# Performance work log

Measured on AMD Instinct MI355X. Metric: run time of the kernel, lower is better.

## Reference

```python
import jax, jax.numpy as jnp
import numpy as np

T, B, IN, H = 256, 128, 512, 1024


def setup_inputs() -> dict:
    key = jax.random.key(0)
    ks = jax.random.split(key, 13)
    s = 1.0 / float(np.sqrt(H))  # torch LSTMCell init: U(-1/sqrt(H), 1/sqrt(H))
    u = lambda k, shp: jax.random.uniform(k, shp, jnp.float32, -s, s)
    return {
        "x": jax.random.normal(ks[0], (T, B, IN), jnp.float32),
        "h0_fwd": jax.random.normal(ks[1], (B, H), jnp.float32),
        "c0_fwd": jax.random.normal(ks[2], (B, H), jnp.float32),
        "h0_rev": jax.random.normal(ks[3], (B, H), jnp.float32),
        "c0_rev": jax.random.normal(ks[4], (B, H), jnp.float32),
        "W_ih_f": u(ks[5], (4 * H, IN)),
        "W_hh_f": u(ks[6], (4 * H, H)),
        "b_ih_f": u(ks[7], (4 * H,)),
        "b_hh_f": u(ks[8], (4 * H,)),
        "W_ih_r": u(ks[9], (4 * H, IN)),
        "W_hh_r": u(ks[10], (4 * H, H)),
        "b_ih_r": u(ks[11], (4 * H,)),
        "b_hh_r": u(ks[12], (4 * H,)),
    }


def _lstm(x, h0, c0, Wih, Whh, bih, bhh, reverse):
    # Precompute the input projection for all timesteps in one big GEMM.
    xp = jnp.einsum('tbi,gi->tbg', x, Wih) + bih + bhh  # [T, B, 4H]

    def step(carry, xg):
        h, c = carry
        gates = xg + h @ Whh.T  # [B, 4H]
        i, f, g, o = jnp.split(gates, 4, axis=-1)  # torch gate order: i, f, g, o
        c = jax.nn.sigmoid(f) * c + jax.nn.sigmoid(i) * jnp.tanh(g)
        h = jax.nn.sigmoid(o) * jnp.tanh(c)
        return (h, c), h

    # reverse=True scans backward in time but emits outputs in original order,
    # exactly matching ReverseLSTMLayer's reverse-process-then-reverse-outputs.
    (h, c), ys = jax.lax.scan(step, (h0, c0), xp, reverse=reverse)
    return ys, h, c


def reference(x, h0_fwd, c0_fwd, h0_rev, c0_rev,
              W_ih_f, W_hh_f, b_ih_f, b_hh_f,
              W_ih_r, W_hh_r, b_ih_r, b_hh_r):
    yf, hf, cf = _lstm(x, h0_fwd, c0_fwd, W_ih_f, W_hh_f, b_ih_f, b_hh_f, False)
    yr, hr, cr = _lstm(x, h0_rev, c0_rev, W_ih_r, W_hh_r, b_ih_r, b_hh_r, True)
    out = jnp.concatenate([yf, yr], axis=-1)  # [T, B, 2H]
    # Faithful to the original's `hidden, cell = output_states` quirk:
    # `hidden` is the forward direction's (h, c) pair stacked,
    # `cell` is the reverse direction's (h, c) pair stacked.
    hidden = jnp.stack([hf, cf])  # [2, B, H]
    cell = jnp.stack([hr, cr])    # [2, B, H]
    return out, (hidden, cell)
```

## Files before the change

### kernel.cpp

```cpp
#include <hip/hip_runtime.h>
#include <hip/hip_bf16.h>

typedef unsigned short u16;
typedef __attribute__((ext_vector_type(8))) short bf16x8;
typedef __attribute__((ext_vector_type(8))) u16   u16x8;
typedef __attribute__((ext_vector_type(4))) float f32x4;

#define T_STEPS 256
#define BATCH   128
#define INDIM   512
#define HDIM    1024
#define GDIM    4096
#define KTOT    1536

#define OFF_XBF   ((size_t)0)
#define XBF_BYTES ((size_t)T_STEPS * BATCH * INDIM * 2)
#define OFF_BM    (OFF_XBF + XBF_BYTES)
#define BM_BYTES  ((size_t)2 * GDIM * KTOT * 2)
#define OFF_BIAS  (OFF_BM + BM_BYTES)
#define BIAS_BYTES ((size_t)2 * GDIM * 4)
#define OFF_CNT   (OFF_BIAS + BIAS_BYTES)
#define OFF_ROLL  (OFF_CNT + 8192)
#define ROLL_BYTES ((size_t)(T_STEPS + 1) * 2 * BATCH * HDIM * 2)
#define WS_NEED   (OFF_ROLL + ROLL_BYTES)


__device__ __forceinline__ u16 f2b(float f) {
  __hip_bfloat16 h = __float2bfloat16(f);
  return *reinterpret_cast<u16*>(&h);
}

__global__ void k_cast_x(const float* __restrict__ x, u16* __restrict__ xs) {
  int i = blockIdx.x * 256 + threadIdx.x;
  int t   = i >> 13;
  int r13 = i & 8191;
  int row = r13 >> 6;
  int c0  = (r13 & 63) * 8;
  int q = row >> 5, rloc = row & 31;
  int mi = rloc >> 4, ar = rloc & 15;
  int kq = c0 >> 7, kr = c0 & 127;
  int ks = kr >> 5, h4 = (kr & 31) >> 3;
  int lane = h4 * 16 + ar;
  const float* src = x + ((size_t)t * BATCH + row) * INDIM + c0;
  f32x4 a = *reinterpret_cast<const f32x4*>(src);
  f32x4 b = *reinterpret_cast<const f32x4*>(src + 4);
  u16x8 u;
  u[0] = f2b(a[0]); u[1] = f2b(a[1]); u[2] = f2b(a[2]); u[3] = f2b(a[3]);
  u[4] = f2b(b[0]); u[5] = f2b(b[1]); u[6] = f2b(b[2]); u[7] = f2b(b[3]);
  size_t dst = ((((((size_t)t * 4 + q) * 4 + kq) * 4 + ks) * 2 + mi) * 64 + lane) * 8;
  *reinterpret_cast<u16x8*>(xs + dst) = u;
}

__global__ void k_build_b(const float* __restrict__ Whh_f, const float* __restrict__ Wih_f,
                          const float* __restrict__ Whh_r, const float* __restrict__ Wih_r,
                          u16* __restrict__ Bm) {
  int blk = blockIdx.x;
  int dir = blk >> 5, jt = blk & 31;
  const float* Whh = dir ? Whh_r : Whh_f;
  const float* Wih = dir ? Wih_r : Wih_f;
  u16* dst = Bm + (size_t)blk * 128 * KTOT;
  for (int c = 0; c < 128; c++) {
    int G = (c >> 5) * HDIM + jt * 32 + (c & 31);
    for (int k = threadIdx.x; k < KTOT; k += 256) {
      float v = (k < HDIM) ? Whh[(size_t)G * HDIM + k] : Wih[(size_t)G * INDIM + (k - HDIM)];
      dst[c * KTOT + k] = f2b(v);
    }
  }
}

__global__ void k_init(const float* __restrict__ h0f, const float* __restrict__ h0r,
                       const float* __restrict__ bihf, const float* __restrict__ bhhf,
                       const float* __restrict__ bihr, const float* __restrict__ bhhr,
                       u16* __restrict__ hfrag, float* __restrict__ bias,
                       unsigned* __restrict__ flags) {
  int i = blockIdx.x * 256 + threadIdx.x;
  if (i < 2 * BATCH * HDIM) {
    int dir = i / (BATCH * HDIM);
    int rem = i - dir * BATCH * HDIM;
    int r = rem / HDIM, c = rem - r * HDIM;
    int q = r >> 5, rloc = r & 31;
    int mi = rloc >> 4, ar = rloc & 15;
    int kq = c >> 8, ks = (c >> 5) & 7, h4 = (c & 31) >> 3, e = c & 7;
    const float* h0 = dir ? h0r : h0f;
    size_t off = ((size_t)(dir * 4 + q)) * 32768
               + (((size_t)(kq * 8 + ks) * 2 + mi) * 64 + h4 * 16 + ar) * 8 + e;
    hfrag[off] = f2b(h0[rem]);
  }
  if (i < 2 * GDIM) {
    int dir = i / GDIM, g = i - dir * GDIM;
    bias[i] = dir ? (bihr[g] + bhhr[g]) : (bihf[g] + bhhf[g]);
  }
  if (i < 512) flags[i] = 0;
}

__global__ __launch_bounds__(512, 2) void k_lstm(
    const u16* __restrict__ xs, const u16* __restrict__ Bm,
    u16* __restrict__ hfrag,
    const float* __restrict__ bias, unsigned* __restrict__ flags,
    const float* __restrict__ c0f, const float* __restrict__ c0r,
    float* __restrict__ out) {
  __shared__ float ldsP[4 * 128 * 37];

  __builtin_amdgcn_fence(__ATOMIC_ACQUIRE, "agent");

  const int wg   = blockIdx.x;
  const int grp  = wg & 7;
  const int dir  = grp >> 2, q = grp & 3;
  const int jt32 = wg >> 3;
  const int tid  = threadIdx.x;
  const int w = tid >> 6, lane = tid & 63;
  const int kq = w >> 1, nh = w & 1;
  const int h4 = lane >> 4, kk = h4 * 8;
  const int ar = lane & 15;

  const u16* bsrc = Bm + (size_t)(dir * 32 + jt32) * 128 * KTOT;
  bf16x8 bh[8][4], bx[4][4];
#pragma unroll
  for (int ks = 0; ks < 8; ks++)
#pragma unroll
    for (int ni = 0; ni < 4; ni++)
      bh[ks][ni] = *reinterpret_cast<const bf16x8*>(
          bsrc + (size_t)(nh * 64 + ni * 16 + ar) * KTOT + 256 * kq + 32 * ks + kk);
#pragma unroll
  for (int ks = 0; ks < 4; ks++)
#pragma unroll
    for (int ni = 0; ni < 4; ni++)
      bx[ks][ni] = *reinterpret_cast<const bf16x8*>(
          bsrc + (size_t)(nh * 64 + ni * 16 + ar) * KTOT + HDIM + 128 * kq + 32 * ks + kk);

  const int rrow = tid >> 4;
  const int jl0  = 2 * (tid & 15);
  const int row0 = q * 32 + rrow;
  const int jg0  = jt32 * 32 + jl0;
  const float* c0 = dir ? c0r : c0f;
  float2 cc = *reinterpret_cast<const float2*>(c0 + (size_t)row0 * HDIM + jg0);
  float cst0 = cc.x, cst1 = cc.y;
  const float2 b_i = *reinterpret_cast<const float2*>(bias + dir * GDIM + 0 * HDIM + jg0);
  const float2 b_f = *reinterpret_cast<const float2*>(bias + dir * GDIM + 1 * HDIM + jg0);
  const float2 b_g = *reinterpret_cast<const float2*>(bias + dir * GDIM + 2 * HDIM + jg0);
  const float2 b_o = *reinterpret_cast<const float2*>(bias + dir * GDIM + 3 * HDIM + jg0);

  const int pmi = rrow >> 4, par = rrow & 15;
  const int ph4 = jl0 >> 3, pe = jl0 & 7;
  const size_t poff = (((size_t)(jt32 * 2 + pmi) * 64 + ph4 * 16 + par) * 8 + pe);

  const unsigned* fpw = flags + grp * 32 + 8 * kq + (lane & 7);

#pragma unroll 1
  for (int s = 0; s < T_STEPS; s++) {
    const int t = dir ? (T_STEPS - 1 - s) : s;

    bf16x8 ax[4][2];
    {
      const u16* xb = xs + ((((size_t)t * 4 + q) * 4 + kq) * 4) * 2 * 512;
#pragma unroll
      for (int ks = 0; ks < 4; ks++)
#pragma unroll
        for (int mi = 0; mi < 2; mi++)
          ax[ks][mi] = *reinterpret_cast<const bf16x8*>(
              xb + ((size_t)(ks * 2 + mi) * 64 + lane) * 8);
    }

    if (s > 0) {
      while (true) {
        unsigned f = __hip_atomic_load(fpw, __ATOMIC_RELAXED, __HIP_MEMORY_SCOPE_AGENT);
        if (__all((int)(f >= (unsigned)s))) break;
        __builtin_amdgcn_s_sleep(1);
      }
      __builtin_amdgcn_sched_barrier(0);
    }

    f32x4 acc[2][4];
#pragma unroll
    for (int mi = 0; mi < 2; mi++)
#pragma unroll
      for (int ni = 0; ni < 4; ni++) acc[mi][ni] = f32x4{0.f, 0.f, 0.f, 0.f};

    const u16* hB = hfrag + ((size_t)s * 8 + dir * 4 + q) * 32768;
#pragma unroll
    for (int half = 0; half < 2; half++) {
      bf16x8 ah[4][2];
#pragma unroll
      for (int k2 = 0; k2 < 4; k2++)
#pragma unroll
        for (int mi = 0; mi < 2; mi++) {
          int ks = half * 4 + k2;
          ah[k2][mi] = *reinterpret_cast<const bf16x8*>(
              hB + (((size_t)(kq * 8 + ks) * 2 + mi) * 64 + lane) * 8);
        }
      if (half == 0) {
#pragma unroll
        for (int ks = 0; ks < 4; ks++)
#pragma unroll
          for (int mi = 0; mi < 2; mi++)
#pragma unroll
            for (int ni = 0; ni < 4; ni++)
              acc[mi][ni] = __builtin_amdgcn_mfma_f32_16x16x32_bf16(ax[ks][mi], bx[ks][ni], acc[mi][ni], 0, 0, 0);
      }
#pragma unroll
      for (int k2 = 0; k2 < 4; k2++)
#pragma unroll
        for (int mi = 0; mi < 2; mi++)
#pragma unroll
          for (int ni = 0; ni < 4; ni++)
            acc[mi][ni] = __builtin_amdgcn_mfma_f32_16x16x32_bf16(
                ah[k2][mi], bh[half * 4 + k2][ni], acc[mi][ni], 0, 0, 0);
    }

    {
      float* pw = ldsP + kq * (128 * 37);
#pragma unroll
      for (int mi = 0; mi < 2; mi++)
#pragma unroll
        for (int ni = 0; ni < 4; ni++) {
          int col = nh * 64 + ni * 16 + ar;
          *reinterpret_cast<f32x4*>(pw + col * 37 + mi * 16 + h4 * 4) = acc[mi][ni];
        }
    }
    __syncthreads();

    float h0v, h1v;
    {
      float gi0 = b_i.x, gi1 = b_i.y, gf0 = b_f.x, gf1 = b_f.y;
      float gg0 = b_g.x, gg1 = b_g.y, go0 = b_o.x, go1 = b_o.y;
#pragma unroll
      for (int k4 = 0; k4 < 4; k4++) {
        const float* p = ldsP + k4 * (128 * 37);
        gi0 += p[(0 * 32 + jl0) * 37 + rrow]; gi1 += p[(0 * 32 + jl0 + 1) * 37 + rrow];
        gf0 += p[(1 * 32 + jl0) * 37 + rrow]; gf1 += p[(1 * 32 + jl0 + 1) * 37 + rrow];
        gg0 += p[(2 * 32 + jl0) * 37 + rrow]; gg1 += p[(2 * 32 + jl0 + 1) * 37 + rrow];
        go0 += p[(3 * 32 + jl0) * 37 + rrow]; go1 += p[(3 * 32 + jl0 + 1) * 37 + rrow];
      }
      float i0 = 1.f / (1.f + __expf(-gi0)), i1 = 1.f / (1.f + __expf(-gi1));
      float f0 = 1.f / (1.f + __expf(-gf0)), f1 = 1.f / (1.f + __expf(-gf1));
      float g0 = tanhf(gg0), g1 = tanhf(gg1);
      float o0 = 1.f / (1.f + __expf(-go0)), o1 = 1.f / (1.f + __expf(-go1));
      cst0 = f0 * cst0 + i0 * g0;
      cst1 = f1 * cst1 + i1 * g1;
      h0v = o0 * tanhf(cst0);
      h1v = o1 * tanhf(cst1);

      unsigned hp = (unsigned)f2b(h0v) | ((unsigned)f2b(h1v) << 16);
      u16* hD = hfrag + ((size_t)(s + 1) * 8 + dir * 4 + q) * 32768;
      __hip_atomic_store(reinterpret_cast<unsigned*>(hD + poff),
                         hp, __ATOMIC_RELAXED, __HIP_MEMORY_SCOPE_AGENT);
    }

    asm volatile("s_waitcnt vmcnt(0)" ::: "memory");
    __syncthreads();
    if (tid == 0)
      __hip_atomic_store(flags + grp * 32 + jt32, (unsigned)(s + 1),
                         __ATOMIC_RELAXED, __HIP_MEMORY_SCOPE_AGENT);

    {
      float2 yv; yv.x = h0v; yv.y = h1v;
      *reinterpret_cast<float2*>(out + ((size_t)t * BATCH + row0) * (2 * HDIM)
                                     + (size_t)dir * HDIM + jg0) = yv;
      if (s == T_STEPS - 1) {
        size_t hid = (size_t)T_STEPS * BATCH * 2 * HDIM;
        size_t base2 = hid + (size_t)dir * 2 * BATCH * HDIM;
        *reinterpret_cast<float2*>(out + base2 + (size_t)row0 * HDIM + jg0) = yv;
        float2 cv; cv.x = cst0; cv.y = cst1;
        *reinterpret_cast<float2*>(out + base2 + (size_t)BATCH * HDIM
                                       + (size_t)row0 * HDIM + jg0) = cv;
      }
    }
  }
}

extern "C" void kernel_launch(void* const* d_in, const int* in_sizes, int n_in,
                              void* d_out, int out_size, void* d_ws, size_t ws_size,
                              hipStream_t stream) {
  const float* x     = (const float*)d_in[0];
  const float* h0f   = (const float*)d_in[1];
  const float* c0f   = (const float*)d_in[2];
  const float* h0r   = (const float*)d_in[3];
  const float* c0r   = (const float*)d_in[4];
  const float* Wih_f = (const float*)d_in[5];
  const float* Whh_f = (const float*)d_in[6];
  const float* bih_f = (const float*)d_in[7];
  const float* bhh_f = (const float*)d_in[8];
  const float* Wih_r = (const float*)d_in[9];
  const float* Whh_r = (const float*)d_in[10];
  const float* bih_r = (const float*)d_in[11];
  const float* bhh_r = (const float*)d_in[12];
  float* out = (float*)d_out;
  char* ws = (char*)d_ws;

  if (ws_size < WS_NEED) return;

  u16* xsf        = (u16*)(ws + OFF_XBF);
  u16* Bm         = (u16*)(ws + OFF_BM);
  float* bias     = (float*)(ws + OFF_BIAS);
  unsigned* flags = (unsigned*)(ws + OFF_CNT);
  u16* hfrag      = (u16*)(ws + OFF_ROLL);

  k_cast_x<<<8192, 256, 0, stream>>>(x, xsf);
  k_build_b<<<64, 256, 0, stream>>>(Whh_f, Wih_f, Whh_r, Wih_r, Bm);
  k_init<<<1024, 256, 0, stream>>>(h0f, h0r, bih_f, bhh_f, bih_r, bhh_r,
                                   hfrag, bias, flags);
  k_lstm<<<256, 512, 0, stream>>>(xsf, Bm, hfrag, bias, flags, c0f, c0r, out);
}
```

Measured before the change: 2.323 ms.

## Retile persistent LSTM to 64-row by 16-column tiles with LDS-resident input weights

Changes the per-workgroup tile from 32 batch rows by 32 hidden units to 64 rows by 16 hidden units, so each direction syncs through two row-groups of 64 workgroups instead of four groups of 32. The x-projection weights move from registers to LDS, and the h fragment loads are double-buffered against the MFMAs. Workgroup-to-XCD mapping is changed so each sync group stays on paired XCDs. The aim is less register pressure, more weight reuse per loaded h fragment, and better overlap of global loads with matrix math. The cost is that each flag wait now covers 64 producers instead of 32, and LDS use is larger.

```diff
diff --git a/kernel.cpp b/kernel.cpp
--- a/kernel.cpp
+++ b/kernel.cpp
@@ -36,18 +36,17 @@
   int r13 = i & 8191;
   int row = r13 >> 6;
   int c0  = (r13 & 63) * 8;
-  int q = row >> 5, rloc = row & 31;
+  int mt = row >> 6, rloc = row & 63;
   int mi = rloc >> 4, ar = rloc & 15;
-  int kq = c0 >> 7, kr = c0 & 127;
-  int ks = kr >> 5, h4 = (kr & 31) >> 3;
-  int lane = h4 * 16 + ar;
+  int kq = c0 >> 7, ksx = (c0 >> 5) & 3, h4 = (c0 & 31) >> 3;
   const float* src = x + ((size_t)t * BATCH + row) * INDIM + c0;
   f32x4 a = *reinterpret_cast<const f32x4*>(src);
   f32x4 b = *reinterpret_cast<const f32x4*>(src + 4);
   u16x8 u;
   u[0] = f2b(a[0]); u[1] = f2b(a[1]); u[2] = f2b(a[2]); u[3] = f2b(a[3]);
   u[4] = f2b(b[0]); u[5] = f2b(b[1]); u[6] = f2b(b[2]); u[7] = f2b(b[3]);
-  size_t dst = ((((((size_t)t * 4 + q) * 4 + kq) * 4 + ks) * 2 + mi) * 64 + lane) * 8;
+  size_t dst = ((size_t)(t * 2 + mt)) * 32768
+             + (((size_t)((kq * 4 + ksx) * 4 + mi)) * 64 + h4 * 16 + ar) * 8;
   *reinterpret_cast<u16x8*>(xs + dst) = u;
 }
 
@@ -55,12 +54,12 @@
                           const float* __restrict__ Whh_r, const float* __restrict__ Wih_r,
                           u16* __restrict__ Bm) {
   int blk = blockIdx.x;
-  int dir = blk >> 5, jt = blk & 31;
+  int dir = blk >> 6, jt = blk & 63;
   const float* Whh = dir ? Whh_r : Whh_f;
   const float* Wih = dir ? Wih_r : Wih_f;
-  u16* dst = Bm + (size_t)blk * 128 * KTOT;
-  for (int c = 0; c < 128; c++) {
-    int G = (c >> 5) * HDIM + jt * 32 + (c & 31);
+  u16* dst = Bm + (size_t)blk * 64 * KTOT;
+  for (int c = 0; c < 64; c++) {
+    int G = (c >> 4) * HDIM + jt * 16 + (c & 15);
     for (int k = threadIdx.x; k < KTOT; k += 256) {
       float v = (k < HDIM) ? Whh[(size_t)G * HDIM + k] : Wih[(size_t)G * INDIM + (k - HDIM)];
       dst[c * KTOT + k] = f2b(v);
@@ -78,12 +77,12 @@
     int dir = i / (BATCH * HDIM);
     int rem = i - dir * BATCH * HDIM;
     int r = rem / HDIM, c = rem - r * HDIM;
-    int q = r >> 5, rloc = r & 31;
+    int mt = r >> 6, rloc = r & 63;
     int mi = rloc >> 4, ar = rloc & 15;
     int kq = c >> 8, ks = (c >> 5) & 7, h4 = (c & 31) >> 3, e = c & 7;
     const float* h0 = dir ? h0r : h0f;
-    size_t off = ((size_t)(dir * 4 + q)) * 32768
-               + (((size_t)(kq * 8 + ks) * 2 + mi) * 64 + h4 * 16 + ar) * 8 + e;
+    size_t off = ((size_t)(dir * 2 + mt)) * 65536
+               + (((size_t)((kq * 8 + ks) * 4 + mi)) * 64 + h4 * 16 + ar) * 8 + e;
     hfrag[off] = f2b(h0[rem]);
   }
   if (i < 2 * GDIM) {
@@ -99,39 +98,45 @@
     const float* __restrict__ bias, unsigned* __restrict__ flags,
     const float* __restrict__ c0f, const float* __restrict__ c0r,
     float* __restrict__ out) {
-  __shared__ float ldsP[4 * 128 * 37];
+  __shared__ char ldsAll[70656 + 65536];
+  float* ldsP = reinterpret_cast<float*>(ldsAll);
+  char* bxl = ldsAll + 70656;
 
   __builtin_amdgcn_fence(__ATOMIC_ACQUIRE, "agent");
 
   const int wg   = blockIdx.x;
-  const int grp  = wg & 7;
-  const int dir  = grp >> 2, q = grp & 3;
-  const int jt32 = wg >> 3;
+  const int xcd  = wg & 7, local = wg >> 3;
+  const int grp  = xcd >> 1;
+  const int dir  = grp >> 1, mt = grp & 1;
+  const int jt   = ((xcd & 1) << 5) | local;
   const int tid  = threadIdx.x;
   const int w = tid >> 6, lane = tid & 63;
   const int kq = w >> 1, nh = w & 1;
   const int h4 = lane >> 4, kk = h4 * 8;
   const int ar = lane & 15;
 
-  const u16* bsrc = Bm + (size_t)(dir * 32 + jt32) * 128 * KTOT;
-  bf16x8 bh[8][4], bx[4][4];
+  const u16* bsrc = Bm + (size_t)(dir * 64 + jt) * 64 * KTOT;
+  bf16x8 bh[8][2];
 #pragma unroll
   for (int ks = 0; ks < 8; ks++)
 #pragma unroll
-    for (int ni = 0; ni < 4; ni++)
+    for (int ni = 0; ni < 2; ni++)
       bh[ks][ni] = *reinterpret_cast<const bf16x8*>(
-          bsrc + (size_t)(nh * 64 + ni * 16 + ar) * KTOT + 256 * kq + 32 * ks + kk);
-#pragma unroll
-  for (int ks = 0; ks < 4; ks++)
-#pragma unroll
-    for (int ni = 0; ni < 4; ni++)
-      bx[ks][ni] = *reinterpret_cast<const bf16x8*>(
-          bsrc + (size_t)(nh * 64 + ni * 16 + ar) * KTOT + HDIM + 128 * kq + 32 * ks + kk);
-
-  const int rrow = tid >> 4;
-  const int jl0  = 2 * (tid & 15);
-  const int row0 = q * 32 + rrow;
-  const int jg0  = jt32 * 32 + jl0;
+          bsrc + (size_t)(nh * 32 + ni * 16 + ar) * KTOT + 256 * kq + 32 * ks + kk);
+
+#pragma unroll
+  for (int i = 0; i < 8; i++) {
+    int fid = i * 8 + w;
+    int kq2 = fid >> 4, ksx2 = (fid >> 2) & 3, nh2 = (fid >> 1) & 1, ni2 = fid & 1;
+    bf16x8 v = *reinterpret_cast<const bf16x8*>(
+        bsrc + (size_t)(nh2 * 32 + ni2 * 16 + ar) * KTOT + HDIM + 128 * kq2 + 32 * ksx2 + kk);
+    *reinterpret_cast<bf16x8*>(bxl + ((size_t)fid * 64 + lane) * 16) = v;
+  }
+
+  const int rrow = tid >> 3;
+  const int jl0  = 2 * (tid & 7);
+  const int row0 = mt * 64 + rrow;
+  const int jg0  = jt * 16 + jl0;
   const float* c0 = dir ? c0r : c0f;
   float2 cc = *reinterpret_cast<const float2*>(c0 + (size_t)row0 * HDIM + jg0);
   float cst0 = cc.x, cst1 = cc.y;
@@ -140,25 +145,26 @@
   const float2 b_g = *reinterpret_cast<const float2*>(bias + dir * GDIM + 2 * HDIM + jg0);
   const float2 b_o = *reinterpret_cast<const float2*>(bias + dir * GDIM + 3 * HDIM + jg0);
 
-  const int pmi = rrow >> 4, par = rrow & 15;
-  const int ph4 = jl0 >> 3, pe = jl0 & 7;
-  const size_t poff = (((size_t)(jt32 * 2 + pmi) * 64 + ph4 * 16 + par) * 8 + pe);
-
-  const unsigned* fpw = flags + grp * 32 + 8 * kq + (lane & 7);
+  const size_t poff = (((size_t)(((jg0 >> 8) * 8 + ((jg0 >> 5) & 7)) * 4 + (rrow >> 4))) * 64
+                       + ((jg0 & 31) >> 3) * 16 + (rrow & 15)) * 8 + (jg0 & 7);
+
+  const unsigned* fpw = flags + grp * 64 + 16 * kq + (lane & 15);
+
+  __syncthreads();
 
 #pragma unroll 1
   for (int s = 0; s < T_STEPS; s++) {
     const int t = dir ? (T_STEPS - 1 - s) : s;
 
-    bf16x8 ax[4][2];
+    bf16x8 ax[4][4];
     {
-      const u16* xb = xs + ((((size_t)t * 4 + q) * 4 + kq) * 4) * 2 * 512;
-#pragma unroll
-      for (int ks = 0; ks < 4; ks++)
-#pragma unroll
-        for (int mi = 0; mi < 2; mi++)
-          ax[ks][mi] = *reinterpret_cast<const bf16x8*>(
-              xb + ((size_t)(ks * 2 + mi) * 64 + lane) * 8);
+      const u16* xb = xs + ((size_t)(t * 2 + mt)) * 32768;
+#pragma unroll
+      for (int ksx = 0; ksx < 4; ksx++)
+#pragma unroll
+        for (int mi = 0; mi < 4; mi++)
+          ax[ksx][mi] = *reinterpret_cast<const bf16x8*>(
+              xb + (((size_t)((kq * 4 + ksx) * 4 + mi)) * 64 + lane) * 8);
     }
 
     if (s > 0) {
@@ -170,51 +176,67 @@
       __builtin_amdgcn_sched_barrier(0);
     }
 
-    f32x4 acc[2][4];
-#pragma unroll
-    for (int mi = 0; mi < 2; mi++)
-#pragma unroll
-      for (int ni = 0; ni < 4; ni++) acc[mi][ni] = f32x4{0.f, 0.f, 0.f, 0.f};
-
-    const u16* hB = hfrag + ((size_t)s * 8 + dir * 4 + q) * 32768;
-#pragma unroll
-    for (int half = 0; half < 2; half++) {
-      bf16x8 ah[4][2];
-#pragma unroll
-      for (int k2 = 0; k2 < 4; k2++)
-#pragma unroll
-        for (int mi = 0; mi < 2; mi++) {
-          int ks = half * 4 + k2;
-          ah[k2][mi] = *reinterpret_cast<const bf16x8*>(
-              hB + (((size_t)(kq * 8 + ks) * 2 + mi) * 64 + lane) * 8);
-        }
-      if (half == 0) {
-#pragma unroll
-        for (int ks = 0; ks < 4; ks++)
-#pragma unroll
-          for (int mi = 0; mi < 2; mi++)
-#pragma unroll
-            for (int ni = 0; ni < 4; ni++)
-              acc[mi][ni] = __builtin_amdgcn_mfma_f32_16x16x32_bf16(ax[ks][mi], bx[ks][ni], acc[mi][ni], 0, 0, 0);
-      }
-#pragma unroll
-      for (int k2 = 0; k2 < 4; k2++)
-#pragma unroll
-        for (int mi = 0; mi < 2; mi++)
-#pragma unroll
-          for (int ni = 0; ni < 4; ni++)
-            acc[mi][ni] = __builtin_amdgcn_mfma_f32_16x16x32_bf16(
-                ah[k2][mi], bh[half * 4 + k2][ni], acc[mi][ni], 0, 0, 0);
-    }
+    f32x4 acc[4][2];
+#pragma unroll
+    for (int mi = 0; mi < 4; mi++)
+#pragma unroll
+      for (int ni = 0; ni < 2; ni++) acc[mi][ni] = f32x4{0.f, 0.f, 0.f, 0.f};
+
+    const u16* hB = hfrag + ((size_t)(s * 4 + dir * 2 + mt)) * 65536;
+    bf16x8 ahA[2][4], ahB[2][4];
+
+#define LOADQ(BUF, G)                                                          \
+  {                                                                            \
+    _Pragma("unroll")                                                          \
+    for (int k2 = 0; k2 < 2; k2++)                                             \
+      _Pragma("unroll")                                                        \
+      for (int mi = 0; mi < 4; mi++)                                           \
+        BUF[k2][mi] = *reinterpret_cast<const bf16x8*>(                        \
+            hB + (((size_t)((kq * 8 + 2 * (G) + k2) * 4 + mi)) * 64 + lane) * 8); \
+  }
+#define MFMAQ(BUF, G)                                                          \
+  {                                                                            \
+    _Pragma("unroll")                                                          \
+    for (int k2 = 0; k2 < 2; k2++)                                             \
+      _Pragma("unroll")                                                        \
+      for (int mi = 0; mi < 4; mi++)                                           \
+        _Pragma("unroll")                                                      \
+        for (int ni = 0; ni < 2; ni++)                                         \
+          acc[mi][ni] = __builtin_amdgcn_mfma_f32_16x16x32_bf16(               \
+              BUF[k2][mi], bh[2 * (G) + k2][ni], acc[mi][ni], 0, 0, 0);        \
+  }
+
+    LOADQ(ahA, 0);
+
+#pragma unroll
+    for (int ksx = 0; ksx < 4; ksx++) {
+      bf16x8 bxf[2];
+#pragma unroll
+      for (int ni = 0; ni < 2; ni++)
+        bxf[ni] = *reinterpret_cast<const bf16x8*>(
+            bxl + (((size_t)(((kq * 4 + ksx) * 2 + nh) * 2 + ni)) * 64 + lane) * 16);
+#pragma unroll
+      for (int mi = 0; mi < 4; mi++)
+#pragma unroll
+        for (int ni = 0; ni < 2; ni++)
+          acc[mi][ni] = __builtin_amdgcn_mfma_f32_16x16x32_bf16(ax[ksx][mi], bxf[ni], acc[mi][ni], 0, 0, 0);
+    }
+
+    LOADQ(ahB, 1); MFMAQ(ahA, 0);
+    LOADQ(ahA, 2); MFMAQ(ahB, 1);
+    LOADQ(ahB, 3); MFMAQ(ahA, 2);
+    MFMAQ(ahB, 3);
+#undef LOADQ
+#undef MFMAQ
 
     {
-      float* pw = ldsP + kq * (128 * 37);
-#pragma unroll
-      for (int mi = 0; mi < 2; mi++)
-#pragma unroll
-        for (int ni = 0; ni < 4; ni++) {
-          int col = nh * 64 + ni * 16 + ar;
-          *reinterpret_cast<f32x4*>(pw + col * 37 + mi * 16 + h4 * 4) = acc[mi][ni];
+      float* pw = ldsP + kq * (64 * 69);
+#pragma unroll
+      for (int mi = 0; mi < 4; mi++)
+#pragma unroll
+        for (int ni = 0; ni < 2; ni++) {
+          int col = nh * 32 + ni * 16 + ar;
+          *reinterpret_cast<f32x4*>(pw + col * 69 + mi * 16 + h4 * 4) = acc[mi][ni];
         }
     }
     __syncthreads();
@@ -225,11 +247,11 @@
       float gg0 = b_g.x, gg1 = b_g.y, go0 = b_o.x, go1 = b_o.y;
 #pragma unroll
       for (int k4 = 0; k4 < 4; k4++) {
-        const float* p = ldsP + k4 * (128 * 37);
-        gi0 += p[(0 * 32 + jl0) * 37 + rrow]; gi1 += p[(0 * 32 + jl0 + 1) * 37 + rrow];
-        gf0 += p[(1 * 32 + jl0) * 37 + rrow]; gf1 += p[(1 * 32 + jl0 + 1) * 37 + rrow];
-        gg0 += p[(2 * 32 + jl0) * 37 + rrow]; gg1 += p[(2 * 32 + jl0 + 1) * 37 + rrow];
-        go0 += p[(3 * 32 + jl0) * 37 + rrow]; go1 += p[(3 * 32 + jl0 + 1) * 37 + rrow];
+        const float* p = ldsP + k4 * (64 * 69);
+        gi0 += p[(0 * 16 + jl0) * 69 + rrow]; gi1 += p[(0 * 16 + jl0 + 1) * 69 + rrow];
+        gf0 += p[(1 * 16 + jl0) * 69 + rrow]; gf1 += p[(1 * 16 + jl0 + 1) * 69 + rrow];
+        gg0 += p[(2 * 16 + jl0) * 69 + rrow]; gg1 += p[(2 * 16 + jl0 + 1) * 69 + rrow];
+        go0 += p[(3 * 16 + jl0) * 69 + rrow]; go1 += p[(3 * 16 + jl0 + 1) * 69 + rrow];
       }
       float i0 = 1.f / (1.f + __expf(-gi0)), i1 = 1.f / (1.f + __expf(-gi1));
       float f0 = 1.f / (1.f + __expf(-gf0)), f1 = 1.f / (1.f + __expf(-gf1));
@@ -241,7 +263,7 @@
       h1v = o1 * tanhf(cst1);
 
       unsigned hp = (unsigned)f2b(h0v) | ((unsigned)f2b(h1v) << 16);
-      u16* hD = hfrag + ((size_t)(s + 1) * 8 + dir * 4 + q) * 32768;
+      u16* hD = hfrag + ((size_t)((s + 1) * 4 + dir * 2 + mt)) * 65536;
       __hip_atomic_store(reinterpret_cast<unsigned*>(hD + poff),
                          hp, __ATOMIC_RELAXED, __HIP_MEMORY_SCOPE_AGENT);
     }
@@ -249,7 +271,7 @@
     asm volatile("s_waitcnt vmcnt(0)" ::: "memory");
     __syncthreads();
     if (tid == 0)
-      __hip_atomic_store(flags + grp * 32 + jt32, (unsigned)(s + 1),
+      __hip_atomic_store(flags + grp * 64 + jt, (unsigned)(s + 1),
                          __ATOMIC_RELAXED, __HIP_MEMORY_SCOPE_AGENT);
 
     {
@@ -296,7 +318,7 @@
   u16* hfrag      = (u16*)(ws + OFF_ROLL);
 
   k_cast_x<<<8192, 256, 0, stream>>>(x, xsf);
-  k_build_b<<<64, 256, 0, stream>>>(Whh_f, Wih_f, Whh_r, Wih_r, Bm);
+  k_build_b<<<128, 256, 0, stream>>>(Whh_f, Wih_f, Whh_r, Wih_r, Bm);
   k_init<<<1024, 256, 0, stream>>>(h0f, h0r, bih_f, bhh_f, bih_r, bhh_r,
                                    hfrag, bias, flags);
   k_lstm<<<256, 512, 0, stream>>>(xsf, Bm, hfrag, bias, flags, c0f, c0r, out);
```

Measured after the change: 2.270 ms. 2.3% less time.
